# Kernel optimization log

Hardware: AMD Instinct MI355X
Metric: run time of the kernel (lower is better)

Reference implementation:

```python
import jax, jax.numpy as jnp
import numpy as np

N_NODES = 100000
N_EDGES = 1600000
D = 128
N_GRAPHS = 128
N_LAYERS = 3


def setup_inputs() -> dict:
    key = jax.random.key(0)
    ks = jax.random.split(key, 3 + 4 * N_LAYERS)
    x = jax.random.normal(ks[0], (N_NODES, D), dtype=jnp.float32)
    edge_index = jax.random.randint(ks[1], (2, N_EDGES), 0, N_NODES, dtype=jnp.int64)
    batch = jnp.sort(jax.random.randint(ks[2], (N_NODES,), 0, N_GRAPHS, dtype=jnp.int64))
    inp = {"x": x, "edge_index": edge_index, "batch": batch}
    scale = 1.0 / np.sqrt(D)
    for l in range(N_LAYERS):
        inp[f"W1_{l}"] = jax.random.normal(ks[3 + 4 * l], (D, D), dtype=jnp.float32) * scale
        inp[f"b1_{l}"] = jnp.zeros((D,), dtype=jnp.float32)
        inp[f"W2_{l}"] = jax.random.normal(ks[4 + 4 * l], (D, D), dtype=jnp.float32) * scale
        inp[f"b2_{l}"] = jnp.zeros((D,), dtype=jnp.float32)
    return inp


def _gin_conv(x, edge_index, W1, b1, W2, b2):
    # GINConv with eps=0: out = MLP(x + sum_{j in N(i)} x_j)
    msgs = x[edge_index[0]]                                   # [E, D] gather
    agg = jax.ops.segment_sum(msgs, edge_index[1], num_segments=N_NODES)
    h = x + agg
    h = jax.nn.relu(h @ W1 + b1)
    return h @ W2 + b2


def reference(x, edge_index, batch,
              W1_0, b1_0, W2_0, b2_0,
              W1_1, b1_1, W2_1, b2_1,
              W1_2, b1_2, W2_2, b2_2):
    params = [(W1_0, b1_0, W2_0, b2_0), (W1_1, b1_1, W2_1, b2_1), (W1_2, b1_2, W2_2, b2_2)]
    h = x
    for l in range(N_LAYERS - 1):
        h = _gin_conv(h, edge_index, *params[l])
        h = jax.nn.relu(h)  # act; dropout with drop_ratio=0 is identity
    node_emb = _gin_conv(h, edge_index, *params[-1])  # JK='last'
    # global_mean_pool
    sums = jax.ops.segment_sum(node_emb, batch, num_segments=N_GRAPHS)
    counts = jax.ops.segment_sum(jnp.ones((N_NODES, 1), node_emb.dtype), batch, num_segments=N_GRAPHS)
    graph_emb = sums / jnp.maximum(counts, 1.0)
    return graph_emb
```

## Files before the change

kernel.cpp:

```cpp
#include <hip/hip_runtime.h>
#include <hip/hip_bf16.h>

#define N_NODES 100000
#define N_PAD   100032
#define N_EDGES 1600000
#define DIM 128
#define N_GRAPHS 128
#define NBKT 98
#define BSTRIDE 18432
#define TILES (N_PAD / 16)
#define GRID_MLP 1024
#define POOL_BLKS ((N_NODES + 127) / 128)

typedef unsigned short u16;
typedef unsigned int u32;
typedef __attribute__((ext_vector_type(8))) short bf16x8;
typedef __attribute__((ext_vector_type(4))) float f32x4;

#define MFMA(A, B, C) __builtin_amdgcn_mfma_f32_16x16x32_bf16(A, B, C, 0, 0, 0)

__device__ __forceinline__ u16 f2bf(float x) {
    u32 u = __float_as_uint(x);
    u = (u + 0x7FFFu + ((u >> 16) & 1u)) >> 16;
    return (u16)u;
}
__device__ __forceinline__ float bf2f(u16 u) {
    return __uint_as_float(((u32)u) << 16);
}

__global__ __launch_bounds__(256) void bucket1_kernel(const int* __restrict__ src,
                                                      const int* __restrict__ dst,
                                                      u32* __restrict__ cursorB,
                                                      u32* __restrict__ pairs) {
    __shared__ int lh[NBKT];
    __shared__ u32 lbase[NBKT];
    int t = threadIdx.x;
    if (t < NBKT) lh[t] = 0;
    __syncthreads();
    int e0 = blockIdx.x * 1024;
    int d[4], s[4], rk[4], bk[4];
#pragma unroll
    for (int k = 0; k < 4; ++k) {
        int e = e0 + t + k * 256;
        if (e < N_EDGES) {
            d[k] = dst[e];
            s[k] = src[e];
            bk[k] = d[k] >> 10;
            rk[k] = atomicAdd(&lh[bk[k]], 1);
        }
    }
    __syncthreads();
    if (t < NBKT) lbase[t] = atomicAdd(&cursorB[t], (u32)lh[t]) + (u32)(t * BSTRIDE);
    __syncthreads();
#pragma unroll
    for (int k = 0; k < 4; ++k) {
        int e = e0 + t + k * 256;
        if (e < N_EDGES) {
            u32 pos = lbase[bk[k]] + (u32)rk[k];
            pairs[pos] = ((u32)(d[k] & 1023) << 22) | (u32)s[k];
        }
    }
}

__global__ __launch_bounds__(1024) void bucket2_kernel(const u32* __restrict__ cursorB,
                                                       const u32* __restrict__ pairs,
                                                       int* __restrict__ row_ptr,
                                                       int* __restrict__ csr) {
    __shared__ int lh[1024];
    __shared__ int rc[1024];
    __shared__ int bs[128];
    int b = blockIdx.x, t = threadIdx.x;

    if (t < 128) bs[t] = (t < NBKT) ? (int)cursorB[t] : 0;
    __syncthreads();
    for (int off = 1; off < 128; off <<= 1) {
        int v = (t < 128 && t >= off) ? bs[t - off] : 0;
        __syncthreads();
        if (t < 128) bs[t] += v;
        __syncthreads();
    }
    int cnt = (int)cursorB[b];
    int bbase = (b == 0) ? 0 : bs[b - 1];

    lh[t] = 0;
    __syncthreads();
    const u32* pb = pairs + (size_t)b * BSTRIDE;
    for (int i = t; i < cnt; i += 1024) atomicAdd(&lh[pb[i] >> 22], 1);
    __syncthreads();

    int own = lh[t];
    for (int off = 1; off < 1024; off <<= 1) {
        int v = (t >= off) ? lh[t - off] : 0;
        __syncthreads();
        lh[t] += v;
        __syncthreads();
    }
    int excl = lh[t] - own;
    int node = b * 1024 + t;
    if (node < N_NODES) row_ptr[node] = bbase + excl;
    if (b == 0 && t == 0) row_ptr[N_NODES] = N_EDGES;
    rc[t] = bbase + excl;
    __syncthreads();

    for (int i = t; i < cnt; i += 1024) {
        u32 p = pb[i];
        int pos = atomicAdd(&rc[p >> 22], 1);
        csr[pos] = (int)(p & 0x3FFFFFu);
    }
}

__global__ __launch_bounds__(256) void xprep_kernel(const float* __restrict__ x,
                                                    u16* __restrict__ hb) {
    int i = blockIdx.x * 256 + threadIdx.x;
    if (i < N_NODES * 32) {
        float4 v = ((const float4*)x)[i];
        ushort4 o;
        o.x = f2bf(v.x); o.y = f2bf(v.y); o.z = f2bf(v.z); o.w = f2bf(v.w);
        ((ushort4*)hb)[i] = o;
    }
}

__global__ __launch_bounds__(256) void agg_kernel(const u16* __restrict__ hb,
                                                  const int* __restrict__ rp,
                                                  const int* __restrict__ csr,
                                                  u16* __restrict__ Ah,
                                                  u16* __restrict__ Al) {
    int node = (blockIdx.x * 256 + threadIdx.x) >> 5;
    int l = threadIdx.x & 31;
    if (node >= N_NODES) return;
    const ushort4* h4 = (const ushort4*)hb;
    ushort4 sv = h4[(size_t)node * 32 + l];
    float a0 = bf2f(sv.x), a1 = bf2f(sv.y), a2 = bf2f(sv.z), a3 = bf2f(sv.w);
    int s = rp[node], e = rp[node + 1];
    int i = s;
    for (; i + 8 <= e; i += 8) {
        ushort4 v0 = h4[(size_t)csr[i + 0] * 32 + l];
        ushort4 v1 = h4[(size_t)csr[i + 1] * 32 + l];
        ushort4 v2 = h4[(size_t)csr[i + 2] * 32 + l];
        ushort4 v3 = h4[(size_t)csr[i + 3] * 32 + l];
        ushort4 v4 = h4[(size_t)csr[i + 4] * 32 + l];
        ushort4 v5 = h4[(size_t)csr[i + 5] * 32 + l];
        ushort4 v6 = h4[(size_t)csr[i + 6] * 32 + l];
        ushort4 v7 = h4[(size_t)csr[i + 7] * 32 + l];
        a0 += ((bf2f(v0.x) + bf2f(v1.x)) + (bf2f(v2.x) + bf2f(v3.x))) +
              ((bf2f(v4.x) + bf2f(v5.x)) + (bf2f(v6.x) + bf2f(v7.x)));
        a1 += ((bf2f(v0.y) + bf2f(v1.y)) + (bf2f(v2.y) + bf2f(v3.y))) +
              ((bf2f(v4.y) + bf2f(v5.y)) + (bf2f(v6.y) + bf2f(v7.y)));
        a2 += ((bf2f(v0.z) + bf2f(v1.z)) + (bf2f(v2.z) + bf2f(v3.z))) +
              ((bf2f(v4.z) + bf2f(v5.z)) + (bf2f(v6.z) + bf2f(v7.z)));
        a3 += ((bf2f(v0.w) + bf2f(v1.w)) + (bf2f(v2.w) + bf2f(v3.w))) +
              ((bf2f(v4.w) + bf2f(v5.w)) + (bf2f(v6.w) + bf2f(v7.w)));
    }
    for (; i < e; ++i) {
        ushort4 v = h4[(size_t)csr[i] * 32 + l];
        a0 += bf2f(v.x); a1 += bf2f(v.y); a2 += bf2f(v.z); a3 += bf2f(v.w);
    }
    ushort4 hv, lv;
    hv.x = f2bf(a0); lv.x = f2bf(a0 - bf2f(hv.x));
    hv.y = f2bf(a1); lv.y = f2bf(a1 - bf2f(hv.y));
    hv.z = f2bf(a2); lv.z = f2bf(a2 - bf2f(hv.z));
    hv.w = f2bf(a3); lv.w = f2bf(a3 - bf2f(hv.w));
    *(ushort4*)(Ah + (size_t)node * 128 + l * 4) = hv;
    *(ushort4*)(Al + (size_t)node * 128 + l * 4) = lv;
}

struct WPrepArgs {
    const float* w[6];
    u16* buf[6];
};
__global__ __launch_bounds__(256) void wprep_kernel(WPrepArgs p) {
    int m = blockIdx.y;
    int idx = blockIdx.x * 256 + threadIdx.x;
    int n = idx >> 7, k = idx & 127;
    float v = p.w[m][k * 128 + n];
    u16 hi = f2bf(v);
    p.buf[m][idx] = hi;
    p.buf[m][idx + 16384] = f2bf(v - bf2f(hi));
}

#define HS 136
__global__ __launch_bounds__(256, 2) void fused_mlp(const u16* __restrict__ Ah,
                                                    const u16* __restrict__ Al,
                                                    const u16* __restrict__ W1,
                                                    const float* __restrict__ b1,
                                                    const u16* __restrict__ W2,
                                                    const float* __restrict__ b2,
                                                    float* __restrict__ Cf,
                                                    u16* __restrict__ Cb, int mode) {
    __shared__ u16 Hh[32 * HS];
    __shared__ u16 Hl[32 * HS];
    int tid = threadIdx.x;
    int lane = tid & 63, wave = tid >> 6;
    int m16 = lane & 15, quad = lane >> 4;
    int colBase = wave * 32;

    bf16x8 W1H[2][4], W1L[2][4], W2H[2][4], W2L[2][4];
#pragma unroll
    for (int nt = 0; nt < 2; ++nt) {
        int n = colBase + nt * 16 + m16;
#pragma unroll
        for (int kb = 0; kb < 4; ++kb) {
            int off = n * 128 + kb * 32 + quad * 8;
            W1H[nt][kb] = *(const bf16x8*)(W1 + off);
            W1L[nt][kb] = *(const bf16x8*)(W1 + off + 16384);
            W2H[nt][kb] = *(const bf16x8*)(W2 + off);
            W2L[nt][kb] = *(const bf16x8*)(W2 + off + 16384);
        }
    }
    float b1v[2][4], b2v[2][4];
#pragma unroll
    for (int nt = 0; nt < 2; ++nt)
#pragma unroll
        for (int rg = 0; rg < 4; ++rg) {
            int col = colBase + nt * 16 + quad * 4 + rg;
            b1v[nt][rg] = b1[col];
            b2v[nt][rg] = b2[col];
        }

    f32x4 z = {0.f, 0.f, 0.f, 0.f};

    for (int t0 = blockIdx.x * 2; t0 < TILES; t0 += 2 * GRID_MLP) {
        bf16x8 aH[2][4], aL[2][4];
#pragma unroll
        for (int p = 0; p < 2; ++p) {
            const u16* ah = Ah + (size_t)((t0 + p) * 16 + m16) * 128 + quad * 8;
            const u16* al = Al + (size_t)((t0 + p) * 16 + m16) * 128 + quad * 8;
#pragma unroll
            for (int kb = 0; kb < 4; ++kb) {
                aH[p][kb] = *(const bf16x8*)(ah + kb * 32);
                aL[p][kb] = *(const bf16x8*)(al + kb * 32);
            }
        }

        f32x4 acc[2][2];
        acc[0][0] = z; acc[0][1] = z; acc[1][0] = z; acc[1][1] = z;

#pragma unroll
        for (int kb = 0; kb < 4; ++kb) {
#pragma unroll
            for (int p = 0; p < 2; ++p) {
                acc[p][0] = MFMA(W1H[0][kb], aH[p][kb], acc[p][0]);
                acc[p][1] = MFMA(W1H[1][kb], aH[p][kb], acc[p][1]);
                acc[p][0] = MFMA(W1H[0][kb], aL[p][kb], acc[p][0]);
                acc[p][1] = MFMA(W1H[1][kb], aL[p][kb], acc[p][1]);
                acc[p][0] = MFMA(W1L[0][kb], aH[p][kb], acc[p][0]);
                acc[p][1] = MFMA(W1L[1][kb], aH[p][kb], acc[p][1]);
            }
        }

        __syncthreads();

#pragma unroll
        for (int p = 0; p < 2; ++p) {
#pragma unroll
            for (int nt = 0; nt < 2; ++nt) {
                ushort4 hv, lv;
#pragma unroll
                for (int rg = 0; rg < 4; ++rg) {
                    float v = fmaxf(acc[p][nt][rg] + b1v[nt][rg], 0.f);
                    u16 hi = f2bf(v);
                    ((u16*)&hv)[rg] = hi;
                    ((u16*)&lv)[rg] = f2bf(v - bf2f(hi));
                }
                int off = (p * 16 + m16) * HS + colBase + nt * 16 + quad * 4;
                *(ushort4*)&Hh[off] = hv;
                *(ushort4*)&Hl[off] = lv;
            }
        }
        __syncthreads();

        acc[0][0] = z; acc[0][1] = z; acc[1][0] = z; acc[1][1] = z;
#pragma unroll
        for (int kb = 0; kb < 4; ++kb) {
#pragma unroll
            for (int p = 0; p < 2; ++p) {
                int off = (p * 16 + m16) * HS + kb * 32 + quad * 8;
                bf16x8 hH = *(const bf16x8*)(&Hh[off]);
                bf16x8 hL = *(const bf16x8*)(&Hl[off]);
                acc[p][0] = MFMA(W2H[0][kb], hH, acc[p][0]);
                acc[p][1] = MFMA(W2H[1][kb], hH, acc[p][1]);
                acc[p][0] = MFMA(W2H[0][kb], hL, acc[p][0]);
                acc[p][1] = MFMA(W2H[1][kb], hL, acc[p][1]);
                acc[p][0] = MFMA(W2L[0][kb], hH, acc[p][0]);
                acc[p][1] = MFMA(W2L[1][kb], hH, acc[p][1]);
            }
        }

#pragma unroll
        for (int p = 0; p < 2; ++p) {
            size_t row = (size_t)((t0 + p) * 16 + m16);
#pragma unroll
            for (int nt = 0; nt < 2; ++nt) {
                int col = colBase + nt * 16 + quad * 4;
                if (mode) {
                    ushort4 o;
#pragma unroll
                    for (int rg = 0; rg < 4; ++rg)
                        ((u16*)&o)[rg] = f2bf(fmaxf(acc[p][nt][rg] + b2v[nt][rg], 0.f));
                    *(ushort4*)(Cb + row * 128 + col) = o;
                } else {
                    float4 o;
                    o.x = acc[p][nt][0] + b2v[nt][0];
                    o.y = acc[p][nt][1] + b2v[nt][1];
                    o.z = acc[p][nt][2] + b2v[nt][2];
                    o.w = acc[p][nt][3] + b2v[nt][3];
                    *(float4*)(Cf + row * 128 + col) = o;
                }
            }
        }
    }
}

__global__ __launch_bounds__(256) void psum_kernel(const float* __restrict__ h,
                                                   const int* __restrict__ batch,
                                                   float* __restrict__ sums) {
    __shared__ int sBatch[128];
    int blk = blockIdx.x, t = threadIdx.x;
    int n0 = blk * 128;
    int nEnd = min(n0 + 128, N_NODES);
    if (t < 128 && n0 + t < N_NODES) sBatch[t] = batch[n0 + t];
    __syncthreads();

    int j = t & 127;
    int half = t >> 7;
    int s = n0 + half * 64;
    int e = min(s + 64, nEnd);

    float acc = 0.f;
    int cur = -1;
    for (int n = s; n < e; ++n) {
        int g = sBatch[n - n0];
        if (g != cur) {
            if (cur >= 0) atomicAdd(&sums[cur * 128 + j], acc);
            cur = g;
            acc = 0.f;
        }
        acc += h[(size_t)n * 128 + j];
    }
    if (cur >= 0) atomicAdd(&sums[cur * 128 + j], acc);
}

__global__ __launch_bounds__(128) void pdiv_kernel(const float* __restrict__ sums,
                                                   const int* __restrict__ batch,
                                                   float* __restrict__ out) {
    __shared__ int sB[2];
    int g = blockIdx.x;
    if (threadIdx.x < 2) {
        int target = g + threadIdx.x;
        int lo = 0, hi = N_NODES;
        while (lo < hi) {
            int m = (lo + hi) >> 1;
            if (batch[m] < target) lo = m + 1; else hi = m;
        }
        sB[threadIdx.x] = lo;
    }
    __syncthreads();
    float cnt = (float)(sB[1] - sB[0]);
    out[g * 128 + threadIdx.x] = sums[g * 128 + threadIdx.x] / fmaxf(cnt, 1.f);
}

extern "C" void kernel_launch(void* const* d_in, const int* in_sizes, int n_in,
                              void* d_out, int out_size, void* d_ws, size_t ws_size,
                              hipStream_t stream) {
    const float* x     = (const float*)d_in[0];
    const int*   ei    = (const int*)d_in[1];
    const int*   batch = (const int*)d_in[2];
    const int*   eSrc  = ei;
    const int*   eDst  = ei + N_EDGES;

    const float* W1[3] = {(const float*)d_in[3], (const float*)d_in[7],  (const float*)d_in[11]};
    const float* b1[3] = {(const float*)d_in[4], (const float*)d_in[8],  (const float*)d_in[12]};
    const float* W2[3] = {(const float*)d_in[5], (const float*)d_in[9],  (const float*)d_in[13]};
    const float* b2[3] = {(const float*)d_in[6], (const float*)d_in[10], (const float*)d_in[14]};

    float* P2 = (float*)d_ws;
    u16*   hb = (u16*)(P2 + (size_t)N_PAD * DIM);
    u16*   Ah = hb + (size_t)N_PAD * DIM;
    u16*   Al = Ah + (size_t)N_PAD * DIM;
    u16*   Wb = Al + (size_t)N_PAD * DIM;
    int*   row_ptr = (int*)(Wb + 6 * 32768);
    u32*   cursorB = (u32*)(row_ptr + N_NODES + 8);
    int*   csr     = (int*)(cursorB + 128);
    float* sums    = (float*)(csr + N_EDGES);
    u32*   pairs   = (u32*)P2;

    hipMemsetAsync(cursorB, 0, 128 * sizeof(u32), stream);
    bucket1_kernel<<<(N_EDGES + 1023) / 1024, 256, 0, stream>>>(eSrc, eDst, cursorB, pairs);
    bucket2_kernel<<<NBKT, 1024, 0, stream>>>(cursorB, pairs, row_ptr, csr);

    xprep_kernel<<<(N_NODES * 32 + 255) / 256, 256, 0, stream>>>(x, hb);
    WPrepArgs wp;
    for (int l = 0; l < 3; ++l) {
        wp.w[2 * l]       = W1[l];
        wp.w[2 * l + 1]   = W2[l];
        wp.buf[2 * l]     = Wb + (size_t)(2 * l) * 32768;
        wp.buf[2 * l + 1] = Wb + (size_t)(2 * l + 1) * 32768;
    }
    wprep_kernel<<<dim3(64, 6), 256, 0, stream>>>(wp);
    hipMemsetAsync(sums, 0, N_GRAPHS * DIM * sizeof(float), stream);

    const int aggGrid = (N_NODES * 32 + 255) / 256;

    for (int l = 0; l < 3; ++l) {
        agg_kernel<<<aggGrid, 256, 0, stream>>>(hb, row_ptr, csr, Ah, Al);
        fused_mlp<<<GRID_MLP, 256, 0, stream>>>(Ah, Al,
                                                Wb + (size_t)(2 * l) * 32768, b1[l],
                                                Wb + (size_t)(2 * l + 1) * 32768, b2[l],
                                                P2, hb, (l < 2) ? 1 : 0);
    }
    psum_kernel<<<POOL_BLKS, 256, 0, stream>>>(P2, batch, sums);
    pdiv_kernel<<<N_GRAPHS, 128, 0, stream>>>(sums, batch, (float*)d_out);
}
```

Measured before the change: 566.4 us.

## Slice node features into 16-column planes for cache-friendly gather aggregation

Stores the bf16 node features and the aggregated hi/lo buffers as 8 column slices of 16 values, each in its own plane, and updates xprep, the MLP loads and the MLP stores to match. The aggregation kernel now processes one slice per block, so the 32-byte gather per neighbour works on a 3.2 MB plane that fits better in cache. Each half-wave processes four edges at a time with lane groups, then combines partial sums with shuffles, and uses nontemporal loads and stores. The cost is eight passes over the CSR and row pointers and narrower 4-byte gathers per lane, which could lower memory-level parallelism.

```diff
diff --git a/kernel.cpp b/kernel.cpp
--- a/kernel.cpp
+++ b/kernel.cpp
@@ -11,6 +11,8 @@
 #define TILES (N_PAD / 16)
 #define GRID_MLP 1024
 #define POOL_BLKS ((N_NODES + 127) / 128)
+#define SSTRIDE ((size_t)N_PAD * 16)
+#define AGG_BPS 391
 
 typedef unsigned short u16;
 typedef unsigned int u32;
@@ -27,6 +29,8 @@
 __device__ __forceinline__ float bf2f(u16 u) {
     return __uint_as_float(((u32)u) << 16);
 }
+__device__ __forceinline__ float bfLo(u32 v) { return __uint_as_float(v << 16); }
+__device__ __forceinline__ float bfHi(u32 v) { return __uint_as_float(v & 0xFFFF0000u); }
 
 __global__ __launch_bounds__(256) void bucket1_kernel(const int* __restrict__ src,
                                                       const int* __restrict__ dst,
@@ -113,10 +117,14 @@
                                                     u16* __restrict__ hb) {
     int i = blockIdx.x * 256 + threadIdx.x;
     if (i < N_NODES * 32) {
+        int node = i >> 5;
+        int cg = i & 31;
         float4 v = ((const float4*)x)[i];
         ushort4 o;
         o.x = f2bf(v.x); o.y = f2bf(v.y); o.z = f2bf(v.z); o.w = f2bf(v.w);
-        ((ushort4*)hb)[i] = o;
+        int slice = cg >> 2;
+        int within = (cg & 3) * 4;
+        *(ushort4*)(hb + (size_t)slice * SSTRIDE + (size_t)node * 16 + within) = o;
     }
 }
 
@@ -125,43 +133,52 @@
                                                   const int* __restrict__ csr,
                                                   u16* __restrict__ Ah,
                                                   u16* __restrict__ Al) {
-    int node = (blockIdx.x * 256 + threadIdx.x) >> 5;
+    int slice = blockIdx.x & 7;
+    int bchunk = blockIdx.x >> 3;
+    int hw = threadIdx.x >> 5;
     int l = threadIdx.x & 31;
-    if (node >= N_NODES) return;
-    const ushort4* h4 = (const ushort4*)hb;
-    ushort4 sv = h4[(size_t)node * 32 + l];
-    float a0 = bf2f(sv.x), a1 = bf2f(sv.y), a2 = bf2f(sv.z), a3 = bf2f(sv.w);
-    int s = rp[node], e = rp[node + 1];
-    int i = s;
-    for (; i + 8 <= e; i += 8) {
-        ushort4 v0 = h4[(size_t)csr[i + 0] * 32 + l];
-        ushort4 v1 = h4[(size_t)csr[i + 1] * 32 + l];
-        ushort4 v2 = h4[(size_t)csr[i + 2] * 32 + l];
-        ushort4 v3 = h4[(size_t)csr[i + 3] * 32 + l];
-        ushort4 v4 = h4[(size_t)csr[i + 4] * 32 + l];
-        ushort4 v5 = h4[(size_t)csr[i + 5] * 32 + l];
-        ushort4 v6 = h4[(size_t)csr[i + 6] * 32 + l];
-        ushort4 v7 = h4[(size_t)csr[i + 7] * 32 + l];
-        a0 += ((bf2f(v0.x) + bf2f(v1.x)) + (bf2f(v2.x) + bf2f(v3.x))) +
-              ((bf2f(v4.x) + bf2f(v5.x)) + (bf2f(v6.x) + bf2f(v7.x)));
-        a1 += ((bf2f(v0.y) + bf2f(v1.y)) + (bf2f(v2.y) + bf2f(v3.y))) +
-              ((bf2f(v4.y) + bf2f(v5.y)) + (bf2f(v6.y) + bf2f(v7.y)));
-        a2 += ((bf2f(v0.z) + bf2f(v1.z)) + (bf2f(v2.z) + bf2f(v3.z))) +
-              ((bf2f(v4.z) + bf2f(v5.z)) + (bf2f(v6.z) + bf2f(v7.z)));
-        a3 += ((bf2f(v0.w) + bf2f(v1.w)) + (bf2f(v2.w) + bf2f(v3.w))) +
-              ((bf2f(v4.w) + bf2f(v5.w)) + (bf2f(v6.w) + bf2f(v7.w)));
-    }
-    for (; i < e; ++i) {
-        ushort4 v = h4[(size_t)csr[i] * 32 + l];
-        a0 += bf2f(v.x); a1 += bf2f(v.y); a2 += bf2f(v.z); a3 += bf2f(v.w);
-    }
-    ushort4 hv, lv;
-    hv.x = f2bf(a0); lv.x = f2bf(a0 - bf2f(hv.x));
-    hv.y = f2bf(a1); lv.y = f2bf(a1 - bf2f(hv.y));
-    hv.z = f2bf(a2); lv.z = f2bf(a2 - bf2f(hv.z));
-    hv.w = f2bf(a3); lv.w = f2bf(a3 - bf2f(hv.w));
-    *(ushort4*)(Ah + (size_t)node * 128 + l * 4) = hv;
-    *(ushort4*)(Al + (size_t)node * 128 + l * 4) = lv;
+    int q = l >> 3;
+    int c = l & 7;
+    const u16* hs = hb + (size_t)slice * SSTRIDE;
+    u16* AhS = Ah + (size_t)slice * SSTRIDE;
+    u16* AlS = Al + (size_t)slice * SSTRIDE;
+    const int strideN = AGG_BPS * 8;
+
+    for (int node = bchunk * 8 + hw; node < N_NODES; node += strideN) {
+        int s = rp[node], e = rp[node + 1];
+        float a0 = 0.f, a1 = 0.f;
+        if (q == 0) {
+            u32 sv = *(const u32*)(hs + (size_t)node * 16 + c * 2);
+            a0 = bfLo(sv); a1 = bfHi(sv);
+        }
+        int i = s;
+        for (; i + 8 <= e; i += 8) {
+            int iA = __builtin_nontemporal_load(csr + i + q);
+            int iB = __builtin_nontemporal_load(csr + i + 4 + q);
+            u32 vA = *(const u32*)(hs + (size_t)iA * 16 + c * 2);
+            u32 vB = *(const u32*)(hs + (size_t)iB * 16 + c * 2);
+            a0 += bfLo(vA) + bfLo(vB);
+            a1 += bfHi(vA) + bfHi(vB);
+        }
+        for (; i < e; i += 4) {
+            if (i + q < e) {
+                int iA = __builtin_nontemporal_load(csr + i + q);
+                u32 vA = *(const u32*)(hs + (size_t)iA * 16 + c * 2);
+                a0 += bfLo(vA);
+                a1 += bfHi(vA);
+            }
+        }
+        a0 += __shfl_xor(a0, 8);  a1 += __shfl_xor(a1, 8);
+        a0 += __shfl_xor(a0, 16); a1 += __shfl_xor(a1, 16);
+        if (q == 0) {
+            u16 h0 = f2bf(a0), h1 = f2bf(a1);
+            u16 l0 = f2bf(a0 - bf2f(h0)), l1 = f2bf(a1 - bf2f(h1));
+            u32 hv = (u32)h0 | ((u32)h1 << 16);
+            u32 lv = (u32)l0 | ((u32)l1 << 16);
+            __builtin_nontemporal_store(hv, (u32*)(AhS + (size_t)node * 16 + c * 2));
+            __builtin_nontemporal_store(lv, (u32*)(AlS + (size_t)node * 16 + c * 2));
+        }
+    }
 }
 
 struct WPrepArgs {
@@ -218,17 +235,18 @@
         }
 
     f32x4 z = {0.f, 0.f, 0.f, 0.f};
+    int within = (quad & 1) * 8;
 
     for (int t0 = blockIdx.x * 2; t0 < TILES; t0 += 2 * GRID_MLP) {
         bf16x8 aH[2][4], aL[2][4];
 #pragma unroll
         for (int p = 0; p < 2; ++p) {
-            const u16* ah = Ah + (size_t)((t0 + p) * 16 + m16) * 128 + quad * 8;
-            const u16* al = Al + (size_t)((t0 + p) * 16 + m16) * 128 + quad * 8;
+            size_t rowOff = (size_t)((t0 + p) * 16 + m16) * 16 + within;
 #pragma unroll
             for (int kb = 0; kb < 4; ++kb) {
-                aH[p][kb] = *(const bf16x8*)(ah + kb * 32);
-                aL[p][kb] = *(const bf16x8*)(al + kb * 32);
+                size_t base = (size_t)(kb * 2 + (quad >> 1)) * SSTRIDE + rowOff;
+                aH[p][kb] = *(const bf16x8*)(Ah + base);
+                aL[p][kb] = *(const bf16x8*)(Al + base);
             }
         }
 
@@ -291,14 +309,14 @@
             size_t row = (size_t)((t0 + p) * 16 + m16);
 #pragma unroll
             for (int nt = 0; nt < 2; ++nt) {
-                int col = colBase + nt * 16 + quad * 4;
                 if (mode) {
                     ushort4 o;
 #pragma unroll
                     for (int rg = 0; rg < 4; ++rg)
                         ((u16*)&o)[rg] = f2bf(fmaxf(acc[p][nt][rg] + b2v[nt][rg], 0.f));
-                    *(ushort4*)(Cb + row * 128 + col) = o;
+                    *(ushort4*)(Cb + (size_t)(wave * 2 + nt) * SSTRIDE + row * 16 + quad * 4) = o;
                 } else {
+                    int col = colBase + nt * 16 + quad * 4;
                     float4 o;
                     o.x = acc[p][nt][0] + b2v[nt][0];
                     o.y = acc[p][nt][1] + b2v[nt][1];
@@ -399,10 +417,8 @@
     wprep_kernel<<<dim3(64, 6), 256, 0, stream>>>(wp);
     hipMemsetAsync(sums, 0, N_GRAPHS * DIM * sizeof(float), stream);
 
-    const int aggGrid = (N_NODES * 32 + 255) / 256;
-
     for (int l = 0; l < 3; ++l) {
-        agg_kernel<<<aggGrid, 256, 0, stream>>>(hb, row_ptr, csr, Ah, Al);
+        agg_kernel<<<AGG_BPS * 8, 256, 0, stream>>>(hb, row_ptr, csr, Ah, Al);
         fused_mlp<<<GRID_MLP, 256, 0, stream>>>(Ah, Al,
                                                 Wb + (size_t)(2 * l) * 32768, b1[l],
                                                 Wb + (size_t)(2 * l + 1) * 32768, b2[l],
```

Measured after the change: 1.007 ms. +77.7%, slower.

## Fuse neighbor aggregation into MLP kernel via shared-memory staging

Applied to the files above, without the earlier changes.

Merges the separate aggregation kernel into the fused MLP kernel. Each block gathers and sums neighbor rows for its 32-node tile directly into shared memory as hi/lo bf16, then runs the MFMA MLP from shared memory. Ping-pong hb buffers avoid read/write hazards between layers. This removes the Ah/Al global round trip and one launch per layer, but the gather now runs in only 1024 blocks at 2 blocks per CU occupancy, holding many weight registers, so latency hiding for the irregular gathers may suffer.

```diff
diff --git a/kernel.cpp b/kernel.cpp
--- a/kernel.cpp
+++ b/kernel.cpp
@@ -118,50 +118,6 @@
         o.x = f2bf(v.x); o.y = f2bf(v.y); o.z = f2bf(v.z); o.w = f2bf(v.w);
         ((ushort4*)hb)[i] = o;
     }
-}
-
-__global__ __launch_bounds__(256) void agg_kernel(const u16* __restrict__ hb,
-                                                  const int* __restrict__ rp,
-                                                  const int* __restrict__ csr,
-                                                  u16* __restrict__ Ah,
-                                                  u16* __restrict__ Al) {
-    int node = (blockIdx.x * 256 + threadIdx.x) >> 5;
-    int l = threadIdx.x & 31;
-    if (node >= N_NODES) return;
-    const ushort4* h4 = (const ushort4*)hb;
-    ushort4 sv = h4[(size_t)node * 32 + l];
-    float a0 = bf2f(sv.x), a1 = bf2f(sv.y), a2 = bf2f(sv.z), a3 = bf2f(sv.w);
-    int s = rp[node], e = rp[node + 1];
-    int i = s;
-    for (; i + 8 <= e; i += 8) {
-        ushort4 v0 = h4[(size_t)csr[i + 0] * 32 + l];
-        ushort4 v1 = h4[(size_t)csr[i + 1] * 32 + l];
-        ushort4 v2 = h4[(size_t)csr[i + 2] * 32 + l];
-        ushort4 v3 = h4[(size_t)csr[i + 3] * 32 + l];
-        ushort4 v4 = h4[(size_t)csr[i + 4] * 32 + l];
-        ushort4 v5 = h4[(size_t)csr[i + 5] * 32 + l];
-        ushort4 v6 = h4[(size_t)csr[i + 6] * 32 + l];
-        ushort4 v7 = h4[(size_t)csr[i + 7] * 32 + l];
-        a0 += ((bf2f(v0.x) + bf2f(v1.x)) + (bf2f(v2.x) + bf2f(v3.x))) +
-              ((bf2f(v4.x) + bf2f(v5.x)) + (bf2f(v6.x) + bf2f(v7.x)));
-        a1 += ((bf2f(v0.y) + bf2f(v1.y)) + (bf2f(v2.y) + bf2f(v3.y))) +
-              ((bf2f(v4.y) + bf2f(v5.y)) + (bf2f(v6.y) + bf2f(v7.y)));
-        a2 += ((bf2f(v0.z) + bf2f(v1.z)) + (bf2f(v2.z) + bf2f(v3.z))) +
-              ((bf2f(v4.z) + bf2f(v5.z)) + (bf2f(v6.z) + bf2f(v7.z)));
-        a3 += ((bf2f(v0.w) + bf2f(v1.w)) + (bf2f(v2.w) + bf2f(v3.w))) +
-              ((bf2f(v4.w) + bf2f(v5.w)) + (bf2f(v6.w) + bf2f(v7.w)));
-    }
-    for (; i < e; ++i) {
-        ushort4 v = h4[(size_t)csr[i] * 32 + l];
-        a0 += bf2f(v.x); a1 += bf2f(v.y); a2 += bf2f(v.z); a3 += bf2f(v.w);
-    }
-    ushort4 hv, lv;
-    hv.x = f2bf(a0); lv.x = f2bf(a0 - bf2f(hv.x));
-    hv.y = f2bf(a1); lv.y = f2bf(a1 - bf2f(hv.y));
-    hv.z = f2bf(a2); lv.z = f2bf(a2 - bf2f(hv.z));
-    hv.w = f2bf(a3); lv.w = f2bf(a3 - bf2f(hv.w));
-    *(ushort4*)(Ah + (size_t)node * 128 + l * 4) = hv;
-    *(ushort4*)(Al + (size_t)node * 128 + l * 4) = lv;
 }
 
 struct WPrepArgs {
@@ -179,20 +135,25 @@
 }
 
 #define HS 136
-__global__ __launch_bounds__(256, 2) void fused_mlp(const u16* __restrict__ Ah,
-                                                    const u16* __restrict__ Al,
-                                                    const u16* __restrict__ W1,
-                                                    const float* __restrict__ b1,
-                                                    const u16* __restrict__ W2,
-                                                    const float* __restrict__ b2,
-                                                    float* __restrict__ Cf,
-                                                    u16* __restrict__ Cb, int mode) {
+__global__ __launch_bounds__(256, 2) void fused_layer(const u16* __restrict__ hbIn,
+                                                      const int* __restrict__ rp,
+                                                      const int* __restrict__ csr,
+                                                      const u16* __restrict__ W1,
+                                                      const float* __restrict__ b1,
+                                                      const u16* __restrict__ W2,
+                                                      const float* __restrict__ b2,
+                                                      float* __restrict__ Cf,
+                                                      u16* __restrict__ Cb, int mode) {
+    __shared__ u16 Ahs[32 * HS];
+    __shared__ u16 Als[32 * HS];
     __shared__ u16 Hh[32 * HS];
     __shared__ u16 Hl[32 * HS];
     int tid = threadIdx.x;
     int lane = tid & 63, wave = tid >> 6;
     int m16 = lane & 15, quad = lane >> 4;
     int colBase = wave * 32;
+    int hw = tid >> 5;
+    int gl = tid & 31;
 
     bf16x8 W1H[2][4], W1L[2][4], W2H[2][4], W2L[2][4];
 #pragma unroll
@@ -218,37 +179,71 @@
         }
 
     f32x4 z = {0.f, 0.f, 0.f, 0.f};
+    const ushort4* h4 = (const ushort4*)hbIn;
 
     for (int t0 = blockIdx.x * 2; t0 < TILES; t0 += 2 * GRID_MLP) {
-        bf16x8 aH[2][4], aL[2][4];
-#pragma unroll
-        for (int p = 0; p < 2; ++p) {
-            const u16* ah = Ah + (size_t)((t0 + p) * 16 + m16) * 128 + quad * 8;
-            const u16* al = Al + (size_t)((t0 + p) * 16 + m16) * 128 + quad * 8;
-#pragma unroll
-            for (int kb = 0; kb < 4; ++kb) {
-                aH[p][kb] = *(const bf16x8*)(ah + kb * 32);
-                aL[p][kb] = *(const bf16x8*)(al + kb * 32);
+        int base = t0 * 16;
+
+#pragma unroll
+        for (int k = 0; k < 4; ++k) {
+            int r = hw + 8 * k;
+            int node = base + r;
+            float a0 = 0.f, a1 = 0.f, a2 = 0.f, a3 = 0.f;
+            if (node < N_NODES) {
+                ushort4 sv = h4[(size_t)node * 32 + gl];
+                a0 = bf2f(sv.x); a1 = bf2f(sv.y); a2 = bf2f(sv.z); a3 = bf2f(sv.w);
+                int s = rp[node], e = rp[node + 1];
+                int i = s;
+                for (; i + 8 <= e; i += 8) {
+                    ushort4 v0 = h4[(size_t)csr[i + 0] * 32 + gl];
+                    ushort4 v1 = h4[(size_t)csr[i + 1] * 32 + gl];
+                    ushort4 v2 = h4[(size_t)csr[i + 2] * 32 + gl];
+                    ushort4 v3 = h4[(size_t)csr[i + 3] * 32 + gl];
+                    ushort4 v4 = h4[(size_t)csr[i + 4] * 32 + gl];
+                    ushort4 v5 = h4[(size_t)csr[i + 5] * 32 + gl];
+                    ushort4 v6 = h4[(size_t)csr[i + 6] * 32 + gl];
+                    ushort4 v7 = h4[(size_t)csr[i + 7] * 32 + gl];
+                    a0 += ((bf2f(v0.x) + bf2f(v1.x)) + (bf2f(v2.x) + bf2f(v3.x))) +
+                          ((bf2f(v4.x) + bf2f(v5.x)) + (bf2f(v6.x) + bf2f(v7.x)));
+                    a1 += ((bf2f(v0.y) + bf2f(v1.y)) + (bf2f(v2.y) + bf2f(v3.y))) +
+                          ((bf2f(v4.y) + bf2f(v5.y)) + (bf2f(v6.y) + bf2f(v7.y)));
+                    a2 += ((bf2f(v0.z) + bf2f(v1.z)) + (bf2f(v2.z) + bf2f(v3.z))) +
+                          ((bf2f(v4.z) + bf2f(v5.z)) + (bf2f(v6.z) + bf2f(v7.z)));
+                    a3 += ((bf2f(v0.w) + bf2f(v1.w)) + (bf2f(v2.w) + bf2f(v3.w))) +
+                          ((bf2f(v4.w) + bf2f(v5.w)) + (bf2f(v6.w) + bf2f(v7.w)));
+                }
+                for (; i < e; ++i) {
+                    ushort4 v = h4[(size_t)csr[i] * 32 + gl];
+                    a0 += bf2f(v.x); a1 += bf2f(v.y); a2 += bf2f(v.z); a3 += bf2f(v.w);
+                }
             }
-        }
+            ushort4 hv, lv;
+            hv.x = f2bf(a0); lv.x = f2bf(a0 - bf2f(hv.x));
+            hv.y = f2bf(a1); lv.y = f2bf(a1 - bf2f(hv.y));
+            hv.z = f2bf(a2); lv.z = f2bf(a2 - bf2f(hv.z));
+            hv.w = f2bf(a3); lv.w = f2bf(a3 - bf2f(hv.w));
+            *(ushort4*)&Ahs[r * HS + gl * 4] = hv;
+            *(ushort4*)&Als[r * HS + gl * 4] = lv;
+        }
+        __syncthreads();
 
         f32x4 acc[2][2];
         acc[0][0] = z; acc[0][1] = z; acc[1][0] = z; acc[1][1] = z;
-
 #pragma unroll
         for (int kb = 0; kb < 4; ++kb) {
 #pragma unroll
             for (int p = 0; p < 2; ++p) {
-                acc[p][0] = MFMA(W1H[0][kb], aH[p][kb], acc[p][0]);
-                acc[p][1] = MFMA(W1H[1][kb], aH[p][kb], acc[p][1]);
-                acc[p][0] = MFMA(W1H[0][kb], aL[p][kb], acc[p][0]);
-                acc[p][1] = MFMA(W1H[1][kb], aL[p][kb], acc[p][1]);
-                acc[p][0] = MFMA(W1L[0][kb], aH[p][kb], acc[p][0]);
-                acc[p][1] = MFMA(W1L[1][kb], aH[p][kb], acc[p][1]);
+                int off = (p * 16 + m16) * HS + kb * 32 + quad * 8;
+                bf16x8 aH = *(const bf16x8*)(&Ahs[off]);
+                bf16x8 aL = *(const bf16x8*)(&Als[off]);
+                acc[p][0] = MFMA(W1H[0][kb], aH, acc[p][0]);
+                acc[p][1] = MFMA(W1H[1][kb], aH, acc[p][1]);
+                acc[p][0] = MFMA(W1H[0][kb], aL, acc[p][0]);
+                acc[p][1] = MFMA(W1H[1][kb], aL, acc[p][1]);
+                acc[p][0] = MFMA(W1L[0][kb], aH, acc[p][0]);
+                acc[p][1] = MFMA(W1L[1][kb], aH, acc[p][1]);
             }
         }
-
-        __syncthreads();
 
 #pragma unroll
         for (int p = 0; p < 2; ++p) {
@@ -288,7 +283,7 @@
 
 #pragma unroll
         for (int p = 0; p < 2; ++p) {
-            size_t row = (size_t)((t0 + p) * 16 + m16);
+            size_t row = (size_t)(base + p * 16 + m16);
 #pragma unroll
             for (int nt = 0; nt < 2; ++nt) {
                 int col = colBase + nt * 16 + quad * 4;
@@ -374,10 +369,9 @@
     const float* b2[3] = {(const float*)d_in[6], (const float*)d_in[10], (const float*)d_in[14]};
 
     float* P2 = (float*)d_ws;
-    u16*   hb = (u16*)(P2 + (size_t)N_PAD * DIM);
-    u16*   Ah = hb + (size_t)N_PAD * DIM;
-    u16*   Al = Ah + (size_t)N_PAD * DIM;
-    u16*   Wb = Al + (size_t)N_PAD * DIM;
+    u16*   hb0 = (u16*)(P2 + (size_t)N_PAD * DIM);
+    u16*   hb1 = hb0 + (size_t)N_PAD * DIM;
+    u16*   Wb  = hb1 + (size_t)N_PAD * DIM;
     int*   row_ptr = (int*)(Wb + 6 * 32768);
     u32*   cursorB = (u32*)(row_ptr + N_NODES + 8);
     int*   csr     = (int*)(cursorB + 128);
@@ -388,7 +382,7 @@
     bucket1_kernel<<<(N_EDGES + 1023) / 1024, 256, 0, stream>>>(eSrc, eDst, cursorB, pairs);
     bucket2_kernel<<<NBKT, 1024, 0, stream>>>(cursorB, pairs, row_ptr, csr);
 
-    xprep_kernel<<<(N_NODES * 32 + 255) / 256, 256, 0, stream>>>(x, hb);
+    xprep_kernel<<<(N_NODES * 32 + 255) / 256, 256, 0, stream>>>(x, hb0);
     WPrepArgs wp;
     for (int l = 0; l < 3; ++l) {
         wp.w[2 * l]       = W1[l];
@@ -399,14 +393,13 @@
     wprep_kernel<<<dim3(64, 6), 256, 0, stream>>>(wp);
     hipMemsetAsync(sums, 0, N_GRAPHS * DIM * sizeof(float), stream);
 
-    const int aggGrid = (N_NODES * 32 + 255) / 256;
-
+    const u16* in[3]  = {hb0, hb1, hb0};
+    u16*       outB[3] = {hb1, hb0, nullptr};
     for (int l = 0; l < 3; ++l) {
-        agg_kernel<<<aggGrid, 256, 0, stream>>>(hb, row_ptr, csr, Ah, Al);
-        fused_mlp<<<GRID_MLP, 256, 0, stream>>>(Ah, Al,
-                                                Wb + (size_t)(2 * l) * 32768, b1[l],
-                                                Wb + (size_t)(2 * l + 1) * 32768, b2[l],
-                                                P2, hb, (l < 2) ? 1 : 0);
+        fused_layer<<<GRID_MLP, 256, 0, stream>>>(in[l], row_ptr, csr,
+                                                  Wb + (size_t)(2 * l) * 32768, b1[l],
+                                                  Wb + (size_t)(2 * l + 1) * 32768, b2[l],
+                                                  P2, outB[l], (l < 2) ? 1 : 0);
     }
     psum_kernel<<<POOL_BLKS, 256, 0, stream>>>(P2, batch, sums);
     pdiv_kernel<<<N_GRAPHS, 128, 0, stream>>>(sums, batch, (float*)d_out);
```

Result: slower. 731.8 us (+29.2%).
